# Optimization experiments

Measured on AMD Instinct MI355X. Metric: run time of the kernel, lower is better.

The kernel has to match this reference:

```python
import jax, jax.numpy as jnp
import numpy as np

N = 50000
E = 800000
D = 128          # in_dim == hidden_dim
EDGE_DIM = 1
H = 128          # hidden_dim


def setup_inputs() -> dict:
    key = jax.random.key(0)
    ks = jax.random.split(key, 16)
    inp = {
        "x": jax.random.normal(ks[0], (N, D), jnp.float32),
        "pos": jax.random.normal(ks[1], (N, 3), jnp.float32),
        "edge_index": jax.random.randint(ks[2], (2, E), 0, N, jnp.int64),
        "edge_attr": jax.random.normal(ks[3], (E, EDGE_DIM), jnp.float32),
        "s": jax.random.uniform(ks[4], (N,), jnp.float32),
    }
    # edge_mlp: Linear(2D+1+edge_dim -> H), SiLU, Linear(H -> H), SiLU
    e_in = 2 * D + 1 + EDGE_DIM
    def lin(k, fan_in, fan_out):
        lim = 1.0 / np.sqrt(fan_in)
        kw, kb = jax.random.split(k)
        W = jax.random.uniform(kw, (fan_in, fan_out), jnp.float32, -lim, lim)
        b = jax.random.uniform(kb, (fan_out,), jnp.float32, -lim, lim)
        return W, b
    inp["W_e1"], inp["b_e1"] = lin(ks[5], e_in, H)
    inp["W_e2"], inp["b_e2"] = lin(ks[6], H, H)
    # node_mlp: Linear(D+H -> H), SiLU, Linear(H -> D)
    inp["W_n1"], inp["b_n1"] = lin(ks[7], D + H, H)
    inp["W_n2"], inp["b_n2"] = lin(ks[8], H, D)
    # coord_mlp: Linear(H -> 1)
    inp["W_c"], inp["b_c"] = lin(ks[9], H, 1)
    return inp


def reference(x, pos, edge_index, edge_attr, s,
              W_e1, b_e1, W_e2, b_e2, W_n1, b_n1, W_n2, b_n2, W_c, b_c):
    src, dst = edge_index[0], edge_index[1]
    n = x.shape[0]

    # edge gather + relative geometry
    diff = pos[dst] - pos[src]                      # [E, 3]
    r2 = jnp.sum(diff * diff, axis=-1, keepdims=True)  # [E, 1]
    e_in = jnp.concatenate([x[dst], x[src], r2, edge_attr], axis=-1)  # [E, 2D+1+edge_dim]

    # edge MLP
    m = jax.nn.silu(e_in @ W_e1 + b_e1)
    m = jax.nn.silu(m @ W_e2 + b_e2)                # [E, H]

    # s-gate on source nodes
    m = m * s[src][:, None]

    # scatter-add aggregation with degree normalization
    m_sum = jax.ops.segment_sum(m, dst, num_segments=n)          # [N, H]
    deg = jax.ops.segment_sum(jnp.ones((m.shape[0], 1), m.dtype), dst, num_segments=n)
    deg = jnp.maximum(deg, 1.0)
    m_sum = m_sum / deg

    # node update
    h = jax.nn.silu(jnp.concatenate([x, m_sum], axis=-1) @ W_n1 + b_n1)
    x_out = h @ W_n2 + b_n2                         # [N, D]

    # coordinate update
    gamma = m @ W_c + b_c                           # [E, 1]
    coord_update = jax.ops.segment_sum(gamma * diff, dst, num_segments=n) / deg
    pos_out = pos + coord_update                    # [N, 3]
    return x_out, pos_out
```

## Files before the change

kernel.cpp:

```cpp
#include <hip/hip_runtime.h>
#include <hip/hip_bf16.h>

#define NN 50000
#define EE 800000
#define SCAN_BLOCKS 196

typedef __bf16 bf16x8_t __attribute__((ext_vector_type(8)));
typedef float f32x4_t __attribute__((ext_vector_type(4)));

__device__ __forceinline__ float silu_f(float v) {
    return v * __builtin_amdgcn_rcpf(1.0f + __expf(-v));
}

__global__ void prep_kernel(const float* __restrict__ x,
                            const float* __restrict__ We1,
                            const float* __restrict__ We2,
                            const float* __restrict__ Wn1,
                            const float* __restrict__ Wn2,
                            const int* __restrict__ eidx,
                            __bf16* __restrict__ xb,
                            __bf16* __restrict__ We1S,
                            __bf16* __restrict__ We2S,
                            __bf16* __restrict__ Wn1T,
                            __bf16* __restrict__ Wn2T,
                            int* __restrict__ hist) {
    int tid = blockIdx.x * blockDim.x + threadIdx.x;
    int np = gridDim.x * blockDim.x;
    const int NX = NN * 128 / 4;
    for (int i = tid; i < NX; i += np) {
        float4 v = ((const float4*)x)[i];
        __bf16* o = xb + (size_t)i * 4;
        o[0] = (__bf16)v.x; o[1] = (__bf16)v.y; o[2] = (__bf16)v.z; o[3] = (__bf16)v.w;
    }
    for (int i = tid; i < 256 * 128; i += np) {
        int k = i >> 7, n = i & 127;
        We1S[(k >> 5) * 4096 + n * 32 + (k & 31)] = (__bf16)We1[i];
        Wn1T[n * 256 + k] = (__bf16)Wn1[i];
    }
    for (int i = tid; i < 128 * 128; i += np) {
        int k = i >> 7, n = i & 127;
        We2S[(k >> 5) * 4096 + n * 32 + (k & 31)] = (__bf16)We2[i];
        Wn2T[n * 128 + k] = (__bf16)Wn2[i];
    }
    for (int i = tid; i < EE; i += np) {
        atomicAdd(&hist[eidx[EE + i]], 1);
    }
}

__global__ void scan_a(const int* __restrict__ hist, int* __restrict__ bsum) {
    __shared__ int sh[256];
    int i = blockIdx.x * 256 + threadIdx.x;
    sh[threadIdx.x] = (i < NN) ? hist[i] : 0;
    __syncthreads();
    for (int s = 128; s > 0; s >>= 1) {
        if (threadIdx.x < s) sh[threadIdx.x] += sh[threadIdx.x + s];
        __syncthreads();
    }
    if (threadIdx.x == 0) bsum[blockIdx.x] = sh[0];
}

__global__ void scan_b(int* __restrict__ bsum) {
    __shared__ int sh[SCAN_BLOCKS];
    int t = threadIdx.x;
    if (t < SCAN_BLOCKS) sh[t] = bsum[t];
    __syncthreads();
    if (t == 0) {
        int acc = 0;
        for (int i = 0; i < SCAN_BLOCKS; ++i) { int v = sh[i]; sh[i] = acc; acc += v; }
    }
    __syncthreads();
    if (t < SCAN_BLOCKS) bsum[t] = sh[t];
}

__global__ void scan_c(const int* __restrict__ hist, const int* __restrict__ bsum,
                       int* __restrict__ off, int* __restrict__ cursor) {
    __shared__ int sh[256];
    int tx = threadIdx.x;
    int i = blockIdx.x * 256 + tx;
    int v = (i < NN) ? hist[i] : 0;
    sh[tx] = v;
    __syncthreads();
    for (int s = 1; s < 256; s <<= 1) {
        int add = (tx >= s) ? sh[tx - s] : 0;
        __syncthreads();
        sh[tx] += add;
        __syncthreads();
    }
    int excl = sh[tx] - v + bsum[blockIdx.x];
    if (i < NN) { off[i] = excl; cursor[i] = excl; }
    if (i == NN - 1) off[NN] = excl + v;
}

__global__ void scatter_kernel(const int* __restrict__ eidx,
                               const float* __restrict__ pos,
                               const float* __restrict__ eattr,
                               const float* __restrict__ s,
                               int* __restrict__ cursor,
                               float4* __restrict__ e_geo,
                               int2* __restrict__ e_nodes,
                               float2* __restrict__ e_gate) {
    int i = blockIdx.x * blockDim.x + threadIdx.x;
    if (i < EE) {
        int si = eidx[i];
        int di = eidx[EE + i];
        int p = atomicAdd(&cursor[di], 1);
        float dx = pos[di * 3 + 0] - pos[si * 3 + 0];
        float dy = pos[di * 3 + 1] - pos[si * 3 + 1];
        float dz = pos[di * 3 + 2] - pos[si * 3 + 2];
        e_geo[p] = make_float4(dx, dy, dz, dx * dx + dy * dy + dz * dz);
        e_nodes[p] = make_int2(si, di);
        e_gate[p] = make_float2(eattr[i], s[si]);
    }
}

__global__ __launch_bounds__(256, 3)
void edge_kernel(const __bf16* __restrict__ xb,
                 const float4* __restrict__ e_geo,
                 const int2* __restrict__ e_nodes,
                 const float2* __restrict__ e_gate,
                 const __bf16* __restrict__ We1S,
                 const float* __restrict__ We1,
                 const float* __restrict__ be1,
                 const __bf16* __restrict__ We2S,
                 const float* __restrict__ be2,
                 const float* __restrict__ Wc,
                 const float* __restrict__ bc,
                 float* __restrict__ msum,
                 float* __restrict__ coordsum) {
    __shared__ __align__(16) __bf16 Wt[128 * 32];
    __shared__ __align__(16) __bf16 A2[128 * 136];
    __shared__ float s_r2[128], s_ea[128], s_sg[128], s_g[128];
    __shared__ float s_diff[128 * 3];
    __shared__ int s_dst[128], s_src[128];

    float* Mf = (float*)A2;

    const int t = threadIdx.x;
    const int e0 = blockIdx.x * 128;
    const int w = t >> 6;
    const int lane = t & 63;
    const int m_ = lane & 15;
    const int q = lane >> 4;

    if (t < 128) {
        float4 g = e_geo[e0 + t];
        int2 nd = e_nodes[e0 + t];
        float2 gt = e_gate[e0 + t];
        s_diff[t * 3 + 0] = g.x; s_diff[t * 3 + 1] = g.y; s_diff[t * 3 + 2] = g.z;
        s_r2[t] = g.w;
        s_ea[t] = gt.x;
        s_sg[t] = gt.y;
        s_src[t] = nd.x;
        s_dst[t] = nd.y;
    }
    __syncthreads();

    const int el0 = w * 16 + m_;
    const int el1 = 64 + w * 16 + m_;
    const int nd0 = s_dst[el0], ns0 = s_src[el0];
    const int nd1 = s_dst[el1], ns1 = s_src[el1];

    f32x4_t acc[2][8];
#pragma unroll
    for (int et = 0; et < 2; ++et)
#pragma unroll
        for (int ot = 0; ot < 8; ++ot) acc[et][ot] = (f32x4_t){0.f, 0.f, 0.f, 0.f};

    const int wrow = t >> 2;
    const int pch = (t & 3) ^ ((wrow >> 1) & 3);
    const int wofs = wrow * 32 + pch * 8;
    const int rofs = m_ * 32 + (q ^ ((m_ >> 1) & 3)) * 8;

    bf16x8_t xf0 = *(const bf16x8_t*)(xb + (long)nd0 * 128 + q * 8);
    bf16x8_t xf1 = *(const bf16x8_t*)(xb + (long)nd1 * 128 + q * 8);
    uint4 v0 = *(const uint4*)(We1S + t * 8);
    uint4 v1 = *(const uint4*)(We1S + 2048 + t * 8);
#pragma unroll
    for (int ks = 0; ks < 8; ++ks) {
        __syncthreads();
        *(uint4*)(Wt + wofs) = v0;
        *(uint4*)(Wt + 64 * 32 + wofs) = v1;
        bf16x8_t nxf0, nxf1;
        uint4 nv0, nv1;
        if (ks < 7) {
            int col = ((ks + 1) & 3) * 32 + q * 8;
            nxf0 = *(const bf16x8_t*)(xb + (long)(ks + 1 < 4 ? nd0 : ns0) * 128 + col);
            nxf1 = *(const bf16x8_t*)(xb + (long)(ks + 1 < 4 ? nd1 : ns1) * 128 + col);
            nv0 = *(const uint4*)(We1S + (ks + 1) * 4096 + t * 8);
            nv1 = *(const uint4*)(We1S + (ks + 1) * 4096 + 2048 + t * 8);
        }
        __syncthreads();
#pragma unroll
        for (int ot = 0; ot < 8; ++ot) {
            bf16x8_t wf = *(const bf16x8_t*)(Wt + ot * (16 * 32) + rofs);
            acc[0][ot] = __builtin_amdgcn_mfma_f32_16x16x32_bf16(wf, xf0, acc[0][ot], 0, 0, 0);
            acc[1][ot] = __builtin_amdgcn_mfma_f32_16x16x32_bf16(wf, xf1, acc[1][ot], 0, 0, 0);
        }
        if (ks < 7) { xf0 = nxf0; xf1 = nxf1; v0 = nv0; v1 = nv1; }
    }

#pragma unroll
    for (int et = 0; et < 2; ++et) {
        int e = et ? el1 : el0;
        float r2 = s_r2[e], ea = s_ea[e];
#pragma unroll
        for (int ot = 0; ot < 8; ++ot) {
            int oc = ot * 16 + q * 4;
            float4 b1 = *(const float4*)(be1 + oc);
            float4 w6 = *(const float4*)(We1 + 256 * 128 + oc);
            float4 w7 = *(const float4*)(We1 + 257 * 128 + oc);
            union { __bf16 h[4]; uint2 u2; } pk;
            pk.h[0] = (__bf16)silu_f(acc[et][ot][0] + b1.x + r2 * w6.x + ea * w7.x);
            pk.h[1] = (__bf16)silu_f(acc[et][ot][1] + b1.y + r2 * w6.y + ea * w7.y);
            pk.h[2] = (__bf16)silu_f(acc[et][ot][2] + b1.z + r2 * w6.z + ea * w7.z);
            pk.h[3] = (__bf16)silu_f(acc[et][ot][3] + b1.w + r2 * w6.w + ea * w7.w);
            *(uint2*)(A2 + e * 136 + oc) = pk.u2;
        }
    }

#pragma unroll
    for (int et = 0; et < 2; ++et)
#pragma unroll
        for (int ot = 0; ot < 8; ++ot) acc[et][ot] = (f32x4_t){0.f, 0.f, 0.f, 0.f};

    uint4 w20 = *(const uint4*)(We2S + t * 8);
    uint4 w21 = *(const uint4*)(We2S + 2048 + t * 8);
    for (int ks = 0; ks < 4; ++ks) {
        __syncthreads();
        *(uint4*)(Wt + wofs) = w20;
        *(uint4*)(Wt + 64 * 32 + wofs) = w21;
        if (ks < 3) {
            w20 = *(const uint4*)(We2S + (ks + 1) * 4096 + t * 8);
            w21 = *(const uint4*)(We2S + (ks + 1) * 4096 + 2048 + t * 8);
        }
        __syncthreads();
        bf16x8_t af0 = *(const bf16x8_t*)(A2 + el0 * 136 + ks * 32 + q * 8);
        bf16x8_t af1 = *(const bf16x8_t*)(A2 + el1 * 136 + ks * 32 + q * 8);
#pragma unroll
        for (int ot = 0; ot < 8; ++ot) {
            bf16x8_t wf = *(const bf16x8_t*)(Wt + ot * (16 * 32) + rofs);
            acc[0][ot] = __builtin_amdgcn_mfma_f32_16x16x32_bf16(wf, af0, acc[0][ot], 0, 0, 0);
            acc[1][ot] = __builtin_amdgcn_mfma_f32_16x16x32_bf16(wf, af1, acc[1][ot], 0, 0, 0);
        }
    }

    {
        float sg0 = s_sg[el0], sg1 = s_sg[el1];
        float gp0 = 0.f, gp1 = 0.f;
#pragma unroll
        for (int ot = 0; ot < 8; ++ot) {
            int oc = ot * 16 + q * 4;
            float4 b2 = *(const float4*)(be2 + oc);
            float4 wc = *(const float4*)(Wc + oc);
            f32x4_t v0_ = acc[0][ot], v1_ = acc[1][ot];
            v0_[0] = silu_f(v0_[0] + b2.x) * sg0; v0_[1] = silu_f(v0_[1] + b2.y) * sg0;
            v0_[2] = silu_f(v0_[2] + b2.z) * sg0; v0_[3] = silu_f(v0_[3] + b2.w) * sg0;
            v1_[0] = silu_f(v1_[0] + b2.x) * sg1; v1_[1] = silu_f(v1_[1] + b2.y) * sg1;
            v1_[2] = silu_f(v1_[2] + b2.z) * sg1; v1_[3] = silu_f(v1_[3] + b2.w) * sg1;
            acc[0][ot] = v0_; acc[1][ot] = v1_;
            gp0 += v0_[0] * wc.x + v0_[1] * wc.y + v0_[2] * wc.z + v0_[3] * wc.w;
            gp1 += v1_[0] * wc.x + v1_[1] * wc.y + v1_[2] * wc.z + v1_[3] * wc.w;
        }
        gp0 += __shfl_xor(gp0, 16); gp0 += __shfl_xor(gp0, 32);
        gp1 += __shfl_xor(gp1, 16); gp1 += __shfl_xor(gp1, 32);
        if (q == 0) {
            float b0 = bc[0];
            s_g[el0] = gp0 + b0;
            s_g[el1] = gp1 + b0;
        }
    }
    __syncthreads();

    if (t < 24) {
        int ax = t % 3, ch = t / 3;
        int base = ch * 16;
        float run = 0.f;
        int cur = s_dst[base];
        for (int r = 0; r < 16; ++r) {
            int rr = base + r;
            int d = s_dst[rr];
            if (d != cur) {
                atomicAdd(&coordsum[cur * 3 + ax], run);
                run = 0.f; cur = d;
            }
            run += s_g[rr] * s_diff[rr * 3 + ax];
        }
        atomicAdd(&coordsum[cur * 3 + ax], run);
    }

#pragma unroll
    for (int ph = 0; ph < 2; ++ph) {
        int lr = w * 16 + m_;
#pragma unroll
        for (int ot = 0; ot < 8; ++ot)
            *(f32x4_t*)(Mf + lr * 132 + ot * 16 + q * 4) = acc[ph][ot];
        __syncthreads();
        {
            int c = t & 127;
            int half = t >> 7;
            int base = ph * 64 + half * 32;
            float run = 0.f;
            int cur = s_dst[base];
            for (int r = 0; r < 32; ++r) {
                int d = s_dst[base + r];
                if (d != cur) {
                    atomicAdd(&msum[(long)cur * 128 + c], run);
                    run = 0.f; cur = d;
                }
                run += Mf[(half * 32 + r) * 132 + c];
            }
            atomicAdd(&msum[(long)cur * 128 + c], run);
        }
        __syncthreads();
    }
}

__global__ __launch_bounds__(256, 2)
void node_kernel(const __bf16* __restrict__ xb,
                 const float* __restrict__ msum,
                 const int* __restrict__ off,
                 const __bf16* __restrict__ Wn1T,
                 const float* __restrict__ bn1,
                 const __bf16* __restrict__ Wn2T,
                 const float* __restrict__ bn2,
                 const float* __restrict__ pos,
                 const float* __restrict__ csum,
                 float* __restrict__ xout,
                 float* __restrict__ pout) {
    __shared__ __align__(16) __bf16 Abf[64 * 264];
    __shared__ __align__(16) __bf16 Wt[128 * 56];
    __shared__ __align__(16) __bf16 A2[64 * 136];

    const int t = threadIdx.x;
    const int r0 = blockIdx.x * 64;
    const int w = t >> 6;
    const int lane = t & 63;
    const int m_ = lane & 15;
    const int q = lane >> 4;

    if (t < 192) {
        int node = r0 + t / 3;
        if (node < NN) {
            int dg = off[node + 1] - off[node];
            float inv = 1.f / (float)(dg < 1 ? 1 : dg);
            int fl = node * 3 + t % 3;
            pout[fl] = pos[fl] + csum[fl] * inv;
        }
    }

    for (int i = 0; i < 8; ++i) {
        int id = t + 256 * i;
        int rl = id >> 5, ch = id & 31;
        int row = r0 + rl;
        int c8 = (ch & 15) * 8;
        union { __bf16 h[8]; uint4 u; } pk;
        if (row < NN) {
            if (ch < 16) {
                pk.u = *(const uint4*)(xb + (long)row * 128 + c8);
            } else {
                const float* mp = msum + (long)row * 128 + c8;
                int dg = off[row + 1] - off[row];
                float inv = 1.f / (float)(dg < 1 ? 1 : dg);
#pragma unroll
                for (int j = 0; j < 8; ++j) pk.h[j] = (__bf16)(mp[j] * inv);
            }
        } else {
            pk.u = make_uint4(0, 0, 0, 0);
        }
        *(uint4*)(Abf + rl * 264 + ((ch < 16) ? 0 : 128) + c8) = pk.u;
    }
    __syncthreads();

    f32x4_t acc[8];
#pragma unroll
    for (int ct = 0; ct < 8; ++ct) acc[ct] = (f32x4_t){0.f, 0.f, 0.f, 0.f};

    for (int ks = 0; ks < 8; ++ks) {
#pragma unroll
        for (int i = 0; i < 2; ++i) {
            int c = t + 256 * i;
            int n = c >> 2, ko = (c & 3) * 8;
            uint4 v = *(const uint4*)(Wn1T + n * 256 + ks * 32 + ko);
            *(uint4*)(Wt + n * 56 + ko) = v;
        }
        __syncthreads();
        bf16x8_t a = *(const bf16x8_t*)(Abf + (w * 16 + m_) * 264 + ks * 32 + q * 8);
#pragma unroll
        for (int ct = 0; ct < 8; ++ct) {
            bf16x8_t b = *(const bf16x8_t*)(Wt + (ct * 16 + m_) * 56 + q * 8);
            acc[ct] = __builtin_amdgcn_mfma_f32_16x16x32_bf16(a, b, acc[ct], 0, 0, 0);
        }
        __syncthreads();
    }
#pragma unroll
    for (int ct = 0; ct < 8; ++ct) {
        int c = ct * 16 + m_;
        float b1 = bn1[c];
#pragma unroll
        for (int r = 0; r < 4; ++r) {
            int el = w * 16 + q * 4 + r;
            float v = acc[ct][r] + b1;
            A2[el * 136 + c] = (__bf16)silu_f(v);
        }
    }
    __syncthreads();

#pragma unroll
    for (int ct = 0; ct < 8; ++ct) acc[ct] = (f32x4_t){0.f, 0.f, 0.f, 0.f};

    for (int ks = 0; ks < 4; ++ks) {
#pragma unroll
        for (int i = 0; i < 2; ++i) {
            int c = t + 256 * i;
            int n = c >> 2, ko = (c & 3) * 8;
            uint4 v = *(const uint4*)(Wn2T + n * 128 + ks * 32 + ko);
            *(uint4*)(Wt + n * 56 + ko) = v;
        }
        __syncthreads();
        bf16x8_t a = *(const bf16x8_t*)(A2 + (w * 16 + m_) * 136 + ks * 32 + q * 8);
#pragma unroll
        for (int ct = 0; ct < 8; ++ct) {
            bf16x8_t b = *(const bf16x8_t*)(Wt + (ct * 16 + m_) * 56 + q * 8);
            acc[ct] = __builtin_amdgcn_mfma_f32_16x16x32_bf16(a, b, acc[ct], 0, 0, 0);
        }
        __syncthreads();
    }
#pragma unroll
    for (int ct = 0; ct < 8; ++ct) {
        int c = ct * 16 + m_;
        float b2 = bn2[c];
#pragma unroll
        for (int r = 0; r < 4; ++r) {
            int el = w * 16 + q * 4 + r;
            int row = r0 + el;
            if (row < NN) xout[(long)row * 128 + c] = acc[ct][r] + b2;
        }
    }
}

extern "C" void kernel_launch(void* const* d_in, const int* in_sizes, int n_in,
                              void* d_out, int out_size, void* d_ws, size_t ws_size,
                              hipStream_t stream) {
    const float* x     = (const float*)d_in[0];
    const float* pos   = (const float*)d_in[1];
    const int*   eidx  = (const int*)d_in[2];
    const float* eattr = (const float*)d_in[3];
    const float* s     = (const float*)d_in[4];
    const float* We1   = (const float*)d_in[5];
    const float* be1   = (const float*)d_in[6];
    const float* We2   = (const float*)d_in[7];
    const float* be2   = (const float*)d_in[8];
    const float* Wn1   = (const float*)d_in[9];
    const float* bn1   = (const float*)d_in[10];
    const float* Wn2   = (const float*)d_in[11];
    const float* bn2   = (const float*)d_in[12];
    const float* Wc    = (const float*)d_in[13];
    const float* bc    = (const float*)d_in[14];

    char* ws = (char*)d_ws;
    __bf16* xb     = (__bf16*)(ws);
    __bf16* We1S   = (__bf16*)(ws + 12800000);
    __bf16* We2S   = (__bf16*)(ws + 12865536);
    __bf16* Wn1T   = (__bf16*)(ws + 12898304);
    __bf16* Wn2T   = (__bf16*)(ws + 12963840);
    float*  msum   = (float*)(ws + 12996608);
    float*  csum   = (float*)(ws + 38596608);
    int*    hist   = (int*)(ws + 39196608);
    int*    off    = (int*)(ws + 39396608);
    int*    cursor = (int*)(ws + 39596672);
    float4* e_geo  = (float4*)(ws + 39796736);
    int2*   e_nodes= (int2*)(ws + 52596736);
    float2* e_gate = (float2*)(ws + 58996736);
    int*    bsum   = (int*)(ws + 65396736);

    float* xout = (float*)d_out;
    float* pout = xout + (size_t)NN * 128;

    hipMemsetAsync(ws + 12996608, 0, 26400000, stream);
    prep_kernel<<<1024, 256, 0, stream>>>(x, We1, We2, Wn1, Wn2, eidx,
                                          xb, We1S, We2S, Wn1T, Wn2T, hist);
    scan_a<<<SCAN_BLOCKS, 256, 0, stream>>>(hist, bsum);
    scan_b<<<1, 256, 0, stream>>>(bsum);
    scan_c<<<SCAN_BLOCKS, 256, 0, stream>>>(hist, bsum, off, cursor);
    scatter_kernel<<<(EE + 255) / 256, 256, 0, stream>>>(eidx, pos, eattr, s, cursor,
                                                         e_geo, e_nodes, e_gate);
    edge_kernel<<<EE / 128, 256, 0, stream>>>(xb, e_geo, e_nodes, e_gate,
                                              We1S, We1, be1, We2S, be2, Wc, bc,
                                              msum, csum);
    node_kernel<<<(NN + 63) / 64, 256, 0, stream>>>(xb, msum, off, Wn1T, bn1, Wn2T, bn2,
                                                    pos, csum, xout, pout);
}
```

Baseline: 406.0 us.

## Precompute per-node first-layer projections and gather them per edge

Splits the first edge-MLP layer by linearity: a new node-level GEMM computes x@W_dst and x@W_src for every node into an fp32 buffer. The edge kernel then gathers and adds these projections instead of running a K=256 MFMA GEMM per edge. This removes most first-layer FLOPs and a weight-staging loop. The cost is a larger fp32 gather per edge (1 KB versus 512 B) and an extra N×256 buffer write.

```diff
diff --git a/kernel.cpp b/kernel.cpp
--- a/kernel.cpp
+++ b/kernel.cpp
@@ -19,7 +19,7 @@
                             const float* __restrict__ Wn2,
                             const int* __restrict__ eidx,
                             __bf16* __restrict__ xb,
-                            __bf16* __restrict__ We1S,
+                            __bf16* __restrict__ WyS,
                             __bf16* __restrict__ We2S,
                             __bf16* __restrict__ Wn1T,
                             __bf16* __restrict__ Wn2T,
@@ -34,7 +34,9 @@
     }
     for (int i = tid; i < 256 * 128; i += np) {
         int k = i >> 7, n = i & 127;
-        We1S[(k >> 5) * 4096 + n * 32 + (k & 31)] = (__bf16)We1[i];
+        int h = (k < 128) ? n : (128 + n);
+        int k2 = k & 127;
+        WyS[(k2 >> 5) * 8192 + h * 32 + (k2 & 31)] = (__bf16)We1[i];
         Wn1T[n * 256 + k] = (__bf16)Wn1[i];
     }
     for (int i = tid; i < 128 * 128; i += np) {
@@ -44,6 +46,76 @@
     }
     for (int i = tid; i < EE; i += np) {
         atomicAdd(&hist[eidx[EE + i]], 1);
+    }
+}
+
+__global__ __launch_bounds__(256, 4)
+void ygemm_kernel(const __bf16* __restrict__ xb,
+                  const __bf16* __restrict__ WyS,
+                  float* __restrict__ y) {
+    __shared__ __align__(16) __bf16 Abf[64 * 136];
+    __shared__ __align__(16) __bf16 Wy[256 * 32];
+
+    const int t = threadIdx.x;
+    const int r0 = blockIdx.x * 64;
+    const int w = t >> 6;
+    const int lane = t & 63;
+    const int m_ = lane & 15;
+    const int q = lane >> 4;
+
+#pragma unroll
+    for (int i = 0; i < 4; ++i) {
+        int id = t + 256 * i;
+        int rl = id >> 4, c8 = (id & 15) * 8;
+        int row = r0 + rl;
+        uint4 v = (row < NN) ? *(const uint4*)(xb + (long)row * 128 + c8)
+                             : make_uint4(0, 0, 0, 0);
+        *(uint4*)(Abf + rl * 136 + c8) = v;
+    }
+
+    f32x4_t acc[16];
+#pragma unroll
+    for (int ct = 0; ct < 16; ++ct) acc[ct] = (f32x4_t){0.f, 0.f, 0.f, 0.f};
+
+    const int wrow = t >> 2;
+    const int pch = (t & 3) ^ ((wrow >> 1) & 3);
+    const int wofs = wrow * 32 + pch * 8;
+    const int rofs = m_ * 32 + (q ^ ((m_ >> 1) & 3)) * 8;
+
+    uint4 v0 = *(const uint4*)(WyS + t * 8);
+    uint4 v1 = *(const uint4*)(WyS + 2048 + t * 8);
+    uint4 v2 = *(const uint4*)(WyS + 4096 + t * 8);
+    uint4 v3 = *(const uint4*)(WyS + 6144 + t * 8);
+#pragma unroll
+    for (int ks = 0; ks < 4; ++ks) {
+        __syncthreads();
+        *(uint4*)(Wy + wofs) = v0;
+        *(uint4*)(Wy + 64 * 32 + wofs) = v1;
+        *(uint4*)(Wy + 128 * 32 + wofs) = v2;
+        *(uint4*)(Wy + 192 * 32 + wofs) = v3;
+        __syncthreads();
+        if (ks < 3) {
+            v0 = *(const uint4*)(WyS + (ks + 1) * 8192 + t * 8);
+            v1 = *(const uint4*)(WyS + (ks + 1) * 8192 + 2048 + t * 8);
+            v2 = *(const uint4*)(WyS + (ks + 1) * 8192 + 4096 + t * 8);
+            v3 = *(const uint4*)(WyS + (ks + 1) * 8192 + 6144 + t * 8);
+        }
+        bf16x8_t a = *(const bf16x8_t*)(Abf + (w * 16 + m_) * 136 + ks * 32 + q * 8);
+#pragma unroll
+        for (int ct = 0; ct < 16; ++ct) {
+            bf16x8_t b = *(const bf16x8_t*)(Wy + ct * (16 * 32) + rofs);
+            acc[ct] = __builtin_amdgcn_mfma_f32_16x16x32_bf16(a, b, acc[ct], 0, 0, 0);
+        }
+    }
+#pragma unroll
+    for (int ct = 0; ct < 16; ++ct) {
+        int c = ct * 16 + m_;
+#pragma unroll
+        for (int r = 0; r < 4; ++r) {
+            int el = w * 16 + q * 4 + r;
+            int row = r0 + el;
+            if (row < NN) y[(long)row * 256 + c] = acc[ct][r];
+        }
     }
 }
 
@@ -114,11 +186,10 @@
 }
 
 __global__ __launch_bounds__(256, 3)
-void edge_kernel(const __bf16* __restrict__ xb,
+void edge_kernel(const float* __restrict__ y,
                  const float4* __restrict__ e_geo,
                  const int2* __restrict__ e_nodes,
                  const float2* __restrict__ e_gate,
-                 const __bf16* __restrict__ We1S,
                  const float* __restrict__ We1,
                  const float* __restrict__ be1,
                  const __bf16* __restrict__ We2S,
@@ -129,9 +200,10 @@
                  float* __restrict__ coordsum) {
     __shared__ __align__(16) __bf16 Wt[128 * 32];
     __shared__ __align__(16) __bf16 A2[128 * 136];
-    __shared__ float s_r2[128], s_ea[128], s_sg[128], s_g[128];
+    __shared__ __align__(16) float4 s_pk[128];
+    __shared__ float s_sg[128], s_g[128];
     __shared__ float s_diff[128 * 3];
-    __shared__ int s_dst[128], s_src[128];
+    __shared__ int s_dst[128];
 
     float* Mf = (float*)A2;
 
@@ -147,18 +219,39 @@
         int2 nd = e_nodes[e0 + t];
         float2 gt = e_gate[e0 + t];
         s_diff[t * 3 + 0] = g.x; s_diff[t * 3 + 1] = g.y; s_diff[t * 3 + 2] = g.z;
-        s_r2[t] = g.w;
-        s_ea[t] = gt.x;
+        s_pk[t] = make_float4(g.w, gt.x, __int_as_float(nd.x), __int_as_float(nd.y));
         s_sg[t] = gt.y;
-        s_src[t] = nd.x;
         s_dst[t] = nd.y;
     }
     __syncthreads();
 
     const int el0 = w * 16 + m_;
     const int el1 = 64 + w * 16 + m_;
-    const int nd0 = s_dst[el0], ns0 = s_src[el0];
-    const int nd1 = s_dst[el1], ns1 = s_src[el1];
+
+    {
+        const int cq = t & 31;
+        const int c4 = cq * 4;
+        const int eb = t >> 5;
+        float4 b1 = *(const float4*)(be1 + c4);
+        float4 w6 = *(const float4*)(We1 + 256 * 128 + c4);
+        float4 w7 = *(const float4*)(We1 + 257 * 128 + c4);
+#pragma unroll 4
+        for (int i = 0; i < 16; ++i) {
+            int e = eb + i * 8;
+            float4 pk4 = s_pk[e];
+            float r2 = pk4.x, ea = pk4.y;
+            int sn = __float_as_int(pk4.z);
+            int dn = __float_as_int(pk4.w);
+            float4 ya = *(const float4*)(y + (long)dn * 256 + c4);
+            float4 yb = *(const float4*)(y + (long)sn * 256 + 128 + c4);
+            union { __bf16 h[4]; uint2 u2; } pk;
+            pk.h[0] = (__bf16)silu_f(ya.x + yb.x + b1.x + r2 * w6.x + ea * w7.x);
+            pk.h[1] = (__bf16)silu_f(ya.y + yb.y + b1.y + r2 * w6.y + ea * w7.y);
+            pk.h[2] = (__bf16)silu_f(ya.z + yb.z + b1.z + r2 * w6.z + ea * w7.z);
+            pk.h[3] = (__bf16)silu_f(ya.w + yb.w + b1.w + r2 * w6.w + ea * w7.w);
+            *(uint2*)(A2 + e * 136 + c4) = pk.u2;
+        }
+    }
 
     f32x4_t acc[2][8];
 #pragma unroll
@@ -171,69 +264,18 @@
     const int wofs = wrow * 32 + pch * 8;
     const int rofs = m_ * 32 + (q ^ ((m_ >> 1) & 3)) * 8;
 
-    bf16x8_t xf0 = *(const bf16x8_t*)(xb + (long)nd0 * 128 + q * 8);
-    bf16x8_t xf1 = *(const bf16x8_t*)(xb + (long)nd1 * 128 + q * 8);
-    uint4 v0 = *(const uint4*)(We1S + t * 8);
-    uint4 v1 = *(const uint4*)(We1S + 2048 + t * 8);
-#pragma unroll
-    for (int ks = 0; ks < 8; ++ks) {
-        __syncthreads();
-        *(uint4*)(Wt + wofs) = v0;
-        *(uint4*)(Wt + 64 * 32 + wofs) = v1;
-        bf16x8_t nxf0, nxf1;
-        uint4 nv0, nv1;
-        if (ks < 7) {
-            int col = ((ks + 1) & 3) * 32 + q * 8;
-            nxf0 = *(const bf16x8_t*)(xb + (long)(ks + 1 < 4 ? nd0 : ns0) * 128 + col);
-            nxf1 = *(const bf16x8_t*)(xb + (long)(ks + 1 < 4 ? nd1 : ns1) * 128 + col);
-            nv0 = *(const uint4*)(We1S + (ks + 1) * 4096 + t * 8);
-            nv1 = *(const uint4*)(We1S + (ks + 1) * 4096 + 2048 + t * 8);
-        }
-        __syncthreads();
-#pragma unroll
-        for (int ot = 0; ot < 8; ++ot) {
-            bf16x8_t wf = *(const bf16x8_t*)(Wt + ot * (16 * 32) + rofs);
-            acc[0][ot] = __builtin_amdgcn_mfma_f32_16x16x32_bf16(wf, xf0, acc[0][ot], 0, 0, 0);
-            acc[1][ot] = __builtin_amdgcn_mfma_f32_16x16x32_bf16(wf, xf1, acc[1][ot], 0, 0, 0);
-        }
-        if (ks < 7) { xf0 = nxf0; xf1 = nxf1; v0 = nv0; v1 = nv1; }
-    }
-
-#pragma unroll
-    for (int et = 0; et < 2; ++et) {
-        int e = et ? el1 : el0;
-        float r2 = s_r2[e], ea = s_ea[e];
-#pragma unroll
-        for (int ot = 0; ot < 8; ++ot) {
-            int oc = ot * 16 + q * 4;
-            float4 b1 = *(const float4*)(be1 + oc);
-            float4 w6 = *(const float4*)(We1 + 256 * 128 + oc);
-            float4 w7 = *(const float4*)(We1 + 257 * 128 + oc);
-            union { __bf16 h[4]; uint2 u2; } pk;
-            pk.h[0] = (__bf16)silu_f(acc[et][ot][0] + b1.x + r2 * w6.x + ea * w7.x);
-            pk.h[1] = (__bf16)silu_f(acc[et][ot][1] + b1.y + r2 * w6.y + ea * w7.y);
-            pk.h[2] = (__bf16)silu_f(acc[et][ot][2] + b1.z + r2 * w6.z + ea * w7.z);
-            pk.h[3] = (__bf16)silu_f(acc[et][ot][3] + b1.w + r2 * w6.w + ea * w7.w);
-            *(uint2*)(A2 + e * 136 + oc) = pk.u2;
-        }
-    }
-
-#pragma unroll
-    for (int et = 0; et < 2; ++et)
-#pragma unroll
-        for (int ot = 0; ot < 8; ++ot) acc[et][ot] = (f32x4_t){0.f, 0.f, 0.f, 0.f};
-
     uint4 w20 = *(const uint4*)(We2S + t * 8);
     uint4 w21 = *(const uint4*)(We2S + 2048 + t * 8);
+#pragma unroll
     for (int ks = 0; ks < 4; ++ks) {
         __syncthreads();
         *(uint4*)(Wt + wofs) = w20;
         *(uint4*)(Wt + 64 * 32 + wofs) = w21;
+        __syncthreads();
         if (ks < 3) {
             w20 = *(const uint4*)(We2S + (ks + 1) * 4096 + t * 8);
             w21 = *(const uint4*)(We2S + (ks + 1) * 4096 + 2048 + t * 8);
         }
-        __syncthreads();
         bf16x8_t af0 = *(const bf16x8_t*)(A2 + el0 * 136 + ks * 32 + q * 8);
         bf16x8_t af1 = *(const bf16x8_t*)(A2 + el1 * 136 + ks * 32 + q * 8);
 #pragma unroll
@@ -459,7 +501,7 @@
 
     char* ws = (char*)d_ws;
     __bf16* xb     = (__bf16*)(ws);
-    __bf16* We1S   = (__bf16*)(ws + 12800000);
+    __bf16* WyS    = (__bf16*)(ws + 12800000);
     __bf16* We2S   = (__bf16*)(ws + 12865536);
     __bf16* Wn1T   = (__bf16*)(ws + 12898304);
     __bf16* Wn2T   = (__bf16*)(ws + 12963840);
@@ -472,20 +514,22 @@
     int2*   e_nodes= (int2*)(ws + 52596736);
     float2* e_gate = (float2*)(ws + 58996736);
     int*    bsum   = (int*)(ws + 65396736);
+    float*  y      = (float*)(ws + 65397760);
 
     float* xout = (float*)d_out;
     float* pout = xout + (size_t)NN * 128;
 
     hipMemsetAsync(ws + 12996608, 0, 26400000, stream);
     prep_kernel<<<1024, 256, 0, stream>>>(x, We1, We2, Wn1, Wn2, eidx,
-                                          xb, We1S, We2S, Wn1T, Wn2T, hist);
+                                          xb, WyS, We2S, Wn1T, Wn2T, hist);
+    ygemm_kernel<<<(NN + 63) / 64, 256, 0, stream>>>(xb, WyS, y);
     scan_a<<<SCAN_BLOCKS, 256, 0, stream>>>(hist, bsum);
     scan_b<<<1, 256, 0, stream>>>(bsum);
     scan_c<<<SCAN_BLOCKS, 256, 0, stream>>>(hist, bsum, off, cursor);
     scatter_kernel<<<(EE + 255) / 256, 256, 0, stream>>>(eidx, pos, eattr, s, cursor,
                                                          e_geo, e_nodes, e_gate);
-    edge_kernel<<<EE / 128, 256, 0, stream>>>(xb, e_geo, e_nodes, e_gate,
-                                              We1S, We1, be1, We2S, be2, Wc, bc,
+    edge_kernel<<<EE / 128, 256, 0, stream>>>(y, e_geo, e_nodes, e_gate,
+                                              We1, be1, We2S, be2, Wc, bc,
                                               msum, csum);
     node_kernel<<<(NN + 63) / 64, 256, 0, stream>>>(xb, msum, off, Wn1T, bn1, Wn2T, bn2,
                                                     pos, csum, xout, pout);
```

Result: no change. 412.1 us (+1.5%).
